# Performance work log

Measured on AMD Instinct MI355X. Metric: run time of the kernel, lower is better.

The kernel has to match this reference:

```python
import jax, jax.numpy as jnp
import numpy as np

ROPE_THETA = 10000.0

def _apply_rope(t):
    # t: [B, H, S, D]; rotate interleaved even/odd pairs
    B, H, S, D = t.shape
    inv_freq = 1.0 / (ROPE_THETA ** (jnp.arange(0, D, 2, dtype=jnp.float32) / D))  # [D/2]
    ang = jnp.arange(S, dtype=jnp.float32)[:, None] * inv_freq[None, :]            # [S, D/2]
    cos = jnp.cos(ang)[None, None]  # [1,1,S,D/2]
    sin = jnp.sin(ang)[None, None]
    te = t[..., 0::2]
    to = t[..., 1::2]
    re = te * cos - to * sin
    ro = te * sin + to * cos
    out = jnp.stack([re, ro], axis=-1).reshape(B, H, S, D)
    return out

def setup_inputs() -> dict:
    key = jax.random.key(0)
    ks = jax.random.split(key, 5)
    B, S, DIM = 2, 2048, 2048
    x = jax.random.normal(ks[0], (B, S, DIM), dtype=jnp.float32)
    scale = 0.02
    Wq = jax.random.normal(ks[1], (DIM, DIM), dtype=jnp.float32) * scale
    Wk = jax.random.normal(ks[2], (DIM, DIM), dtype=jnp.float32) * scale
    Wv = jax.random.normal(ks[3], (DIM, DIM), dtype=jnp.float32) * scale
    Wo = jax.random.normal(ks[4], (DIM, DIM), dtype=jnp.float32) * scale
    return {"x": x, "Wq": Wq, "Wk": Wk, "Wv": Wv, "Wo": Wo}

def reference(x, Wq, Wk, Wv, Wo):
    B, S, DIM = x.shape
    H = 16
    HD = DIM // H
    # nn.Linear(bias=False) with weight [out,in]: y = x @ W.T; here W stored [in,out]
    q = (x @ Wq).reshape(B, S, H, HD).transpose(0, 2, 1, 3)  # [B,H,S,HD]
    k = (x @ Wk).reshape(B, S, H, HD).transpose(0, 2, 1, 3)
    v = (x @ Wv).reshape(B, S, H, HD).transpose(0, 2, 1, 3)
    q = _apply_rope(q)
    k = _apply_rope(k)
    scores = jnp.einsum('bhqd,bhkd->bhqk', q, k) / jnp.sqrt(jnp.float32(HD))  # [B,H,S,S]
    causal = jnp.tril(jnp.ones((S, S), dtype=bool))
    scores = jnp.where(causal[None, None], scores, jnp.float32(-jnp.inf))
    attn = jax.nn.softmax(scores, axis=-1)
    out = jnp.einsum('bhqk,bhkd->bhqd', attn, v)            # [B,H,S,HD]
    out = out.transpose(0, 2, 1, 3).reshape(B, S, DIM)
    return out @ Wo  # output projection (dropout is identity in eval)
```

## Files before the change

### kernel.cpp

```cpp
#include <hip/hip_runtime.h>
#include <hip/hip_bf16.h>
#include <math.h>

typedef __bf16 bf16;
typedef __attribute__((ext_vector_type(2))) __bf16 bf16x2;
typedef __attribute__((ext_vector_type(4))) __bf16 bf16x4;
typedef __attribute__((ext_vector_type(8))) __bf16 bf16x8;
typedef __attribute__((ext_vector_type(4))) float f32x4;

#define LDS_ASYNC16(gptr, lptr)                                                        \
  __builtin_amdgcn_global_load_lds(                                                    \
      (const __attribute__((address_space(1))) void*)(gptr),                           \
      (__attribute__((address_space(3))) void*)(lptr), 16, 0, 0)

constexpr int BATCH = 2, SEQ = 2048, DIM = 2048, NH = 16, HD = 128;
constexpr float QSC = 0.12751744f;
constexpr float FREQC = 0.20762050593046f;

template <int CTRL>
__device__ __forceinline__ float dpp_mov_f(float x) {
  return __int_as_float(__builtin_amdgcn_update_dpp(
      __float_as_int(x), __float_as_int(x), CTRL, 0xf, 0xf, false));
}
__device__ __forceinline__ float rowmax16(float x) {
  x = fmaxf(x, dpp_mov_f<0x121>(x));
  x = fmaxf(x, dpp_mov_f<0x122>(x));
  x = fmaxf(x, dpp_mov_f<0x124>(x));
  x = fmaxf(x, dpp_mov_f<0x128>(x));
  return x;
}
__device__ __forceinline__ float rowsum16(float x) {
  x += dpp_mov_f<0x121>(x);
  x += dpp_mov_f<0x122>(x);
  x += dpp_mov_f<0x124>(x);
  x += dpp_mov_f<0x128>(x);
  return x;
}

__global__ void cvt_f32_to_bf16(const float4* __restrict__ in,
                                bf16x4* __restrict__ out, int n4) {
  int i = blockIdx.x * blockDim.x + threadIdx.x;
  if (i >= n4) return;
  float4 v = in[i];
  bf16x4 o;
  o[0] = (bf16)v.x; o[1] = (bf16)v.y; o[2] = (bf16)v.z; o[3] = (bf16)v.w;
  out[i] = o;
}

__global__ void transpose_w4(const float* __restrict__ W0, const float* __restrict__ W1,
                             const float* __restrict__ W2, const float* __restrict__ W3,
                             bf16* __restrict__ T0, bf16* __restrict__ T3) {
  __shared__ float tile[32][33];
  const int z = blockIdx.z;
  const float* W = (z == 0) ? W0 : (z == 1) ? W1 : (z == 2) ? W2 : W3;
  bf16* WT = (z == 3) ? T3 : (T0 + (size_t)z * DIM * DIM);
  int tx = threadIdx.x, ty = threadIdx.y;
  int bx = blockIdx.x * 32, by = blockIdx.y * 32;
#pragma unroll
  for (int j = 0; j < 32; j += 8)
    tile[ty + j][tx] = W[(size_t)(by + ty + j) * DIM + bx + tx];
  __syncthreads();
#pragma unroll
  for (int j = 0; j < 32; j += 8)
    WT[(size_t)(bx + ty + j) * DIM + by + tx] = (bf16)tile[tx][ty + j];
}

__device__ __forceinline__ void stage_half(const bf16* __restrict__ src, int g0, int ks,
                                           bf16* lds, int w, int lane) {
#pragma unroll
  for (int j = 0; j < 2; ++j) {
    const int u = (j * 8 + w) * 64 + lane;
    const int row = u >> 2;
    const int kc = (u & 3) ^ ((u >> 3) & 3);
    LDS_ASYNC16(src + (size_t)(g0 + row) * DIM + ks + kc * 8,
                lds + (size_t)((j * 8 + w) * 64) * 8);
  }
}

__global__ __launch_bounds__(512) void gemm_qkv(const bf16* __restrict__ A,
                                                const bf16* __restrict__ BT,
                                                bf16* __restrict__ Qb,
                                                bf16* __restrict__ Kb,
                                                bf16* __restrict__ VTo) {
  constexpr int RSZ = 256 * 32;
  constexpr int NT = DIM / 64;
  __shared__ __attribute__((aligned(16))) bf16 As[4 * RSZ];
  __shared__ __attribute__((aligned(16))) bf16 Bs[4 * RSZ];
  const int tid = threadIdx.x;
  const int w = tid >> 6, lane = tid & 63;
  const int quad = lane >> 4, ln = lane & 15;
  const int wm = w >> 2, wn = w & 3;
  const int lb = blockIdx.x;
  const int wgid = (lb & 7) * 48 + (lb >> 3);
  const int bx = wgid % 24, by = wgid / 24;
  const int m0 = by * 256, n0 = bx * 256;
  const int pc = (quad ^ ((ln >> 1) & 3)) * 8;
  const int aoff = wm * 128 + ln;
  const int boff = wn * 64 + ln;

  f32x4 acc[8][4] = {};

  stage_half(A,  m0, 0,  As + 0 * RSZ, w, lane);
  stage_half(BT, n0, 0,  Bs + 0 * RSZ, w, lane);
  stage_half(A,  m0, 32, As + 1 * RSZ, w, lane);
  stage_half(BT, n0, 32, Bs + 1 * RSZ, w, lane);
  stage_half(A,  m0, 64, As + 2 * RSZ, w, lane);
  stage_half(BT, n0, 64, Bs + 2 * RSZ, w, lane);
  stage_half(BT, n0, 96, Bs + 3 * RSZ, w, lane);
  asm volatile("s_waitcnt vmcnt(6)" ::: "memory");
  __builtin_amdgcn_s_barrier();

#pragma unroll 2
  for (int t = 0; t < NT; ++t) {
    const int b2 = (t & 1) * 2;
    const bf16* Ab0 = As + b2 * RSZ;
    const bf16* Ab1 = Ab0 + RSZ;
    const bf16* Bb0 = Bs + b2 * RSZ;
    const bf16* Bb1 = Bb0 + RSZ;
    bf16x8 af[4], bfr[4];

#pragma unroll
    for (int i = 0; i < 4; ++i)
      af[i] = *(const bf16x8*)(Ab0 + (aoff + i * 16) * 32 + pc);
#pragma unroll
    for (int i = 0; i < 4; ++i)
      bfr[i] = *(const bf16x8*)(Bb0 + (boff + i * 16) * 32 + pc);
    if (t + 1 < NT)
      stage_half(A, m0, (t + 1) * 64 + 32, As + ((((t + 1) & 1) * 2) + 1) * RSZ, w, lane);
    __builtin_amdgcn_s_barrier();
    asm volatile("s_waitcnt lgkmcnt(0)" ::: "memory");
    __builtin_amdgcn_s_setprio(1);
#pragma unroll
    for (int mf = 0; mf < 4; ++mf)
#pragma unroll
      for (int nf = 0; nf < 4; ++nf)
        acc[mf][nf] = __builtin_amdgcn_mfma_f32_16x16x32_bf16(
            af[mf], bfr[nf], acc[mf][nf], 0, 0, 0);
    __builtin_amdgcn_s_setprio(0);
    __builtin_amdgcn_s_barrier();

#pragma unroll
    for (int i = 0; i < 4; ++i)
      af[i] = *(const bf16x8*)(Ab0 + (aoff + 64 + i * 16) * 32 + pc);
    if (t + 2 < NT)
      stage_half(BT, n0, (t + 2) * 64, Bs + b2 * RSZ, w, lane);
    __builtin_amdgcn_s_barrier();
    asm volatile("s_waitcnt lgkmcnt(0)" ::: "memory");
    __builtin_amdgcn_s_setprio(1);
#pragma unroll
    for (int mf = 0; mf < 4; ++mf)
#pragma unroll
      for (int nf = 0; nf < 4; ++nf)
        acc[4 + mf][nf] = __builtin_amdgcn_mfma_f32_16x16x32_bf16(
            af[mf], bfr[nf], acc[4 + mf][nf], 0, 0, 0);
    __builtin_amdgcn_s_setprio(0);
    __builtin_amdgcn_s_barrier();

#pragma unroll
    for (int i = 0; i < 4; ++i)
      af[i] = *(const bf16x8*)(Ab1 + (aoff + i * 16) * 32 + pc);
#pragma unroll
    for (int i = 0; i < 4; ++i)
      bfr[i] = *(const bf16x8*)(Bb1 + (boff + i * 16) * 32 + pc);
    if (t + 2 < NT)
      stage_half(A, m0, (t + 2) * 64, As + b2 * RSZ, w, lane);
    __builtin_amdgcn_s_barrier();
    asm volatile("s_waitcnt lgkmcnt(0)" ::: "memory");
    __builtin_amdgcn_s_setprio(1);
#pragma unroll
    for (int mf = 0; mf < 4; ++mf)
#pragma unroll
      for (int nf = 0; nf < 4; ++nf)
        acc[mf][nf] = __builtin_amdgcn_mfma_f32_16x16x32_bf16(
            af[mf], bfr[nf], acc[mf][nf], 0, 0, 0);
    __builtin_amdgcn_s_setprio(0);
    __builtin_amdgcn_s_barrier();

#pragma unroll
    for (int i = 0; i < 4; ++i)
      af[i] = *(const bf16x8*)(Ab1 + (aoff + 64 + i * 16) * 32 + pc);
    if (t + 2 < NT)
      stage_half(BT, n0, (t + 2) * 64 + 32, Bs + (b2 + 1) * RSZ, w, lane);
    __builtin_amdgcn_s_barrier();
    asm volatile("s_waitcnt lgkmcnt(0)" ::: "memory");
    __builtin_amdgcn_s_setprio(1);
#pragma unroll
    for (int mf = 0; mf < 4; ++mf)
#pragma unroll
      for (int nf = 0; nf < 4; ++nf)
        acc[4 + mf][nf] = __builtin_amdgcn_mfma_f32_16x16x32_bf16(
            af[mf], bfr[nf], acc[4 + mf][nf], 0, 0, 0);
    __builtin_amdgcn_s_setprio(0);
    if (t + 2 < NT) asm volatile("s_waitcnt vmcnt(6)" ::: "memory");
    else            asm volatile("s_waitcnt vmcnt(0)" ::: "memory");
    __builtin_amdgcn_s_barrier();
  }

  const int sel = n0 >> 11;
  if (sel == 2) {
#pragma unroll
    for (int mf = 0; mf < 8; ++mf)
#pragma unroll
      for (int nf = 0; nf < 4; ++nf) {
        int gr = m0 + wm * 128 + mf * 16 + quad * 4;
        int fc = (n0 + wn * 64 + nf * 16 + ln) & 2047;
        int bb = gr >> 11, s0 = gr & (SEQ - 1);
        int h = fc >> 7, d = fc & (HD - 1);
        bf16x4 pk;
#pragma unroll
        for (int r = 0; r < 4; ++r) pk[r] = (bf16)acc[mf][nf][r];
        *(bf16x4*)(VTo + ((size_t)((bb * NH + h) * HD + d)) * SEQ + s0) = pk;
      }
  } else {
    bf16* Dst = sel ? Kb : Qb;
    const float osc = sel ? 1.0f : QSC;
#pragma unroll
    for (int nf = 0; nf < 4; ++nf) {
      int gc = n0 + wn * 64 + nf * 16 + ln;
      int fc = gc & 2047, d = fc & (HD - 1);
      float freq = exp2f(-(float)(d >> 1) * FREQC);
      bool ev = !(d & 1);
#pragma unroll
      for (int mf = 0; mf < 8; ++mf) {
#pragma unroll
        for (int r = 0; r < 4; ++r) {
          int gr = m0 + wm * 128 + mf * 16 + quad * 4 + r;
          int s = gr & (SEQ - 1);
          float ang = (float)s * freq;
          float sn, cs;
          __sincosf(ang, &sn, &cs);
          float own = acc[mf][nf][r];
          float oth = __shfl_xor(own, 1);
          float res = ev ? (own * cs - oth * sn) : (oth * sn + own * cs);
          Dst[(size_t)gr * DIM + fc] = (bf16)(res * osc);
        }
      }
    }
  }
}

template <int MODE>
__global__ __launch_bounds__(256) void gemm_bt(const bf16* __restrict__ A,
                                               const bf16* __restrict__ BT,
                                               void* __restrict__ C) {
  __shared__ __attribute__((aligned(16))) bf16 As[128 * 64];
  __shared__ __attribute__((aligned(16))) bf16 Bs[128 * 64];
  const int tid = threadIdx.x;
  const int w = tid >> 6, lane = tid & 63;
  const int quad = lane >> 4, ln = lane & 15;
  const int m0 = blockIdx.y * 128, n0 = blockIdx.x * 128;
  const int wm = (w >> 1) * 64, wn = (w & 1) * 64;
  const int l7 = ln & 7;
  f32x4 acc[4][4] = {};

  for (int k0 = 0; k0 < DIM; k0 += 64) {
#pragma unroll
    for (int i = 0; i < 4; ++i) {
      const int c = i * 256 + tid;
      const int row = c >> 3, p = c & 7;
      LDS_ASYNC16(A  + (size_t)(m0 + row) * DIM + k0 + ((p ^ (row & 7)) * 8),
                  As + (size_t)(i * 256 + w * 64) * 8);
      LDS_ASYNC16(BT + (size_t)(n0 + row) * DIM + k0 + ((p ^ (row & 7)) * 8),
                  Bs + (size_t)(i * 256 + w * 64) * 8);
    }
    __syncthreads();
#pragma unroll
    for (int kh = 0; kh < 2; ++kh) {
      bf16x8 af[4], bfr[4];
#pragma unroll
      for (int t = 0; t < 4; ++t)
        af[t] = *(const bf16x8*)(As + (wm + t * 16 + ln) * 64 +
                                 (((kh * 4 + quad) ^ l7) * 8));
#pragma unroll
      for (int t = 0; t < 4; ++t)
        bfr[t] = *(const bf16x8*)(Bs + (wn + t * 16 + ln) * 64 +
                                  (((kh * 4 + quad) ^ l7) * 8));
#pragma unroll
      for (int mt = 0; mt < 4; ++mt)
#pragma unroll
        for (int nt = 0; nt < 4; ++nt)
          acc[mt][nt] = __builtin_amdgcn_mfma_f32_16x16x32_bf16(
              af[mt], bfr[nt], acc[mt][nt], 0, 0, 0);
    }
    __syncthreads();
  }

  if (MODE == 0) {
    bf16* Co = (bf16*)C;
#pragma unroll
    for (int mt = 0; mt < 4; ++mt)
#pragma unroll
      for (int nt = 0; nt < 4; ++nt) {
        int gr = m0 + wm + mt * 16 + quad * 4;
        int gc = n0 + wn + nt * 16 + ln;
#pragma unroll
        for (int r = 0; r < 4; ++r)
          Co[(size_t)(gr + r) * DIM + gc] = (bf16)acc[mt][nt][r];
      }
  } else {
    float* Co = (float*)C;
#pragma unroll
    for (int mt = 0; mt < 4; ++mt)
#pragma unroll
      for (int nt = 0; nt < 4; ++nt) {
        int gr = m0 + wm + mt * 16 + quad * 4;
        int gc = n0 + wn + nt * 16 + ln;
#pragma unroll
        for (int r = 0; r < 4; ++r)
          Co[(size_t)(gr + r) * DIM + gc] = acc[mt][nt][r];
      }
  }
}

__device__ __forceinline__ int ml_off(int t) {
  return (t < 10) ? 2 * (t - 5) : (t < 15) ? 10 + 3 * (t - 10) : 25;
}
__device__ __forceinline__ int op_off(int t) {
  return (t < 10) ? (t - 5) : (t < 15) ? 5 + 2 * (t - 10) : 15;
}

constexpr int PSTR = 72;
__global__ __launch_bounds__(256) void flash_attn(
    const bf16* __restrict__ Q, const bf16* __restrict__ K,
    const bf16* __restrict__ VT, bf16* __restrict__ O,
    bf16* __restrict__ Opart, float* __restrict__ Mpart,
    float* __restrict__ Lpart) {
  __shared__ __attribute__((aligned(16))) bf16 Ks[64 * 128];
  __shared__ __attribute__((aligned(16))) bf16 VTs[128 * 64];
  __shared__ __attribute__((aligned(16))) bf16 Ps[4][32 * PSTR];
  const int tid = threadIdx.x;
  const int w = tid >> 6, lane = tid & 63, quad = lane >> 4, ln = lane & 15;
  const int lb = blockIdx.x;
  const int low3 = lb & 7, rest = lb >> 3;
  const int e = rest % 34;
  const int bh = (rest / 34) * 8 + low3;
  int t, c0, nc;
  if (e < 5)       { t = e;                  c0 = 0;               nc = 1; }
  else if (e < 15) { t = 5 + ((e - 5) >> 1); c0 = (e - 5) & 1;     nc = 2; }
  else if (e < 30) { int q = (e - 15) / 3;   t = 10 + q; c0 = (e - 15) - 3 * q; nc = 3; }
  else             { t = 15;                 c0 = e - 30;          nc = 4; }
  const int q0 = t * 128;
  const int ktN = 2 * (t + 1);
  const int kt0 = c0 * 10;
  const int kt1 = min(kt0 + 10, ktN);
  const bool chunked = (nc > 1);
  const int b = bh >> 4, h = bh & 15;

  bf16x8 qf[2][4];
#pragma unroll
  for (int mt = 0; mt < 2; ++mt)
#pragma unroll
    for (int kc = 0; kc < 4; ++kc)
      qf[mt][kc] = *(const bf16x8*)(Q + ((size_t)b * SEQ + q0 + w * 32 + mt * 16 + ln) * DIM +
                                    h * HD + kc * 32 + quad * 8);
  f32x4 o[2][8] = {};
  float mst[2][4], lst[2][4];
#pragma unroll
  for (int mt = 0; mt < 2; ++mt)
#pragma unroll
    for (int r = 0; r < 4; ++r) { mst[mt][r] = -1e30f; lst[mt][r] = 0.f; }

  for (int kt = kt0; kt < kt1; ++kt) {
    __syncthreads();
#pragma unroll
    for (int i = 0; i < 4; ++i) {
      const int c = i * 256 + tid;
      LDS_ASYNC16(K + ((size_t)b * SEQ + kt * 64 + (c >> 4)) * DIM + h * HD +
                      (((c & 15) ^ ((c >> 4) & 15)) * 8),
                  Ks + (size_t)(i * 256 + w * 64) * 8);
      LDS_ASYNC16(VT + ((size_t)((b * NH + h) * HD) + (c >> 3)) * SEQ + kt * 64 +
                      (((c & 7) ^ ((c >> 3) & 7)) * 8),
                  VTs + (size_t)(i * 256 + w * 64) * 8);
    }
    __syncthreads();

    f32x4 s[2][4] = {};
#pragma unroll
    for (int nt = 0; nt < 4; ++nt) {
      bf16x8 kf[4];
#pragma unroll
      for (int kc = 0; kc < 4; ++kc)
        kf[kc] = *(const bf16x8*)(Ks + (nt * 16 + ln) * 128 +
                                  (((kc * 4 + quad) ^ ln) * 8));
#pragma unroll
      for (int kc = 0; kc < 4; ++kc)
#pragma unroll
        for (int mt = 0; mt < 2; ++mt)
          s[mt][nt] = __builtin_amdgcn_mfma_f32_16x16x32_bf16(
              qf[mt][kc], kf[kc], s[mt][nt], 0, 0, 0);
    }

    const bool diag = (kt * 64 + 63 > q0);
    if (diag) {
#pragma unroll
      for (int mt = 0; mt < 2; ++mt)
#pragma unroll
        for (int nt = 0; nt < 4; ++nt)
#pragma unroll
          for (int r = 0; r < 4; ++r) {
            int kg = kt * 64 + nt * 16 + ln;
            int qg = q0 + w * 32 + mt * 16 + quad * 4 + r;
            if (kg > qg) s[mt][nt][r] = -1e30f;
          }
    }

#pragma unroll
    for (int mt = 0; mt < 2; ++mt)
#pragma unroll
      for (int r = 0; r < 4; ++r) {
        float rm = fmaxf(fmaxf(s[mt][0][r], s[mt][1][r]),
                         fmaxf(s[mt][2][r], s[mt][3][r]));
        rm = rowmax16(rm);
        float mold = mst[mt][r];
        float mnew = fmaxf(mold, rm);
        float alpha = exp2f(mold - mnew);
        mst[mt][r] = mnew;
        float rs = 0.f;
#pragma unroll
        for (int nt = 0; nt < 4; ++nt) {
          float p = exp2f(s[mt][nt][r] - mnew);
          rs += p;
          Ps[w][(mt * 16 + quad * 4 + r) * PSTR + nt * 16 + ln] = (bf16)p;
        }
        lst[mt][r] = lst[mt][r] * alpha + rs;
#pragma unroll
        for (int nd = 0; nd < 8; ++nd) o[mt][nd][r] *= alpha;
      }
    __syncthreads();

#pragma unroll
    for (int kc2 = 0; kc2 < 2; ++kc2) {
      bf16x8 pf[2];
#pragma unroll
      for (int mt = 0; mt < 2; ++mt)
        pf[mt] = *(const bf16x8*)(&Ps[w][(mt * 16 + ln) * PSTR + kc2 * 32 + quad * 8]);
#pragma unroll
      for (int nd = 0; nd < 8; ++nd) {
        bf16x8 vf = *(const bf16x8*)(VTs + (nd * 16 + ln) * 64 +
                                     (((kc2 * 4 + quad) ^ (ln & 7)) * 8));
#pragma unroll
        for (int mt = 0; mt < 2; ++mt)
          o[mt][nd] = __builtin_amdgcn_mfma_f32_16x16x32_bf16(
              pf[mt], vf, o[mt][nd], 0, 0, 0);
      }
    }
  }

  if (!chunked) {
#pragma unroll
    for (int mt = 0; mt < 2; ++mt)
#pragma unroll
      for (int r = 0; r < 4; ++r) {
        float inv = 1.f / rowsum16(lst[mt][r]);
        int qg = q0 + w * 32 + mt * 16 + quad * 4 + r;
#pragma unroll
        for (int nd = 0; nd < 8; ++nd)
          O[((size_t)b * SEQ + qg) * DIM + h * HD + nd * 16 + ln] =
              (bf16)(o[mt][nd][r] * inv);
      }
  } else {
    const int mls = bh * 29 + ml_off(t) + c0;
    bf16* Op = (c0 == 0) ? nullptr
                         : Opart + (size_t)(bh * 18 + op_off(t) + (c0 - 1)) * (128 * 128);
#pragma unroll
    for (int mt = 0; mt < 2; ++mt)
#pragma unroll
      for (int r = 0; r < 4; ++r) {
        float l = rowsum16(lst[mt][r]);
        int qr = w * 32 + mt * 16 + quad * 4 + r;
        if (ln == 0) {
          Mpart[mls * 128 + qr] = mst[mt][r];
          Lpart[mls * 128 + qr] = l;
        }
        if (c0 == 0) {
#pragma unroll
          for (int nd = 0; nd < 8; ++nd)
            O[((size_t)b * SEQ + q0 + qr) * DIM + h * HD + nd * 16 + ln] =
                (bf16)o[mt][nd][r];
        } else {
#pragma unroll
          for (int nd = 0; nd < 8; ++nd)
            Op[qr * 128 + nd * 16 + ln] = (bf16)o[mt][nd][r];
        }
      }
  }
}

__global__ __launch_bounds__(256) void flash_merge(const bf16* __restrict__ Opart,
                                                   const float* __restrict__ Mpart,
                                                   const float* __restrict__ Lpart,
                                                   bf16* __restrict__ O) {
  const int bh = blockIdx.x;
  const int t = 5 + blockIdx.y;
  const int nc = (t < 10) ? 2 : (t < 15) ? 3 : 4;
  const int b = bh >> 4, h = bh & 15;
  const int row = threadIdx.x >> 1, half = threadIdx.x & 1;
  const int mlb = bh * 29 + ml_off(t);
  float m[4], l[4], wt[4];
  float M = -1e30f;
  for (int c = 0; c < nc; ++c) {
    m[c] = Mpart[(mlb + c) * 128 + row];
    l[c] = Lpart[(mlb + c) * 128 + row];
    M = fmaxf(M, m[c]);
  }
  float wsum = 0.f;
  for (int c = 0; c < nc; ++c) { wt[c] = exp2f(m[c] - M); wsum += wt[c] * l[c]; }
  const float inv = 1.f / wsum;
  bf16* dst = O + ((size_t)b * SEQ + t * 128 + row) * DIM + h * HD + half * 64;
  const bf16* pb = Opart + (size_t)(bh * 18 + op_off(t)) * (128 * 128) + row * 128 + half * 64;
#pragma unroll
  for (int j = 0; j < 8; ++j) {
    bf16x8 a0 = *(const bf16x8*)(dst + j * 8);
    float acc[8];
#pragma unroll
    for (int k = 0; k < 8; ++k) acc[k] = wt[0] * (float)a0[k];
    for (int c = 1; c < nc; ++c) {
      bf16x8 a = *(const bf16x8*)(pb + (size_t)(c - 1) * (128 * 128) + j * 8);
#pragma unroll
      for (int k = 0; k < 8; ++k) acc[k] += wt[c] * (float)a[k];
    }
    bf16x8 o8;
#pragma unroll
    for (int k = 0; k < 8; ++k) o8[k] = (bf16)(acc[k] * inv);
    *(bf16x8*)(dst + j * 8) = o8;
  }
}

extern "C" void kernel_launch(void* const* d_in, const int* in_sizes, int n_in,
                              void* d_out, int out_size, void* d_ws, size_t ws_size,
                              hipStream_t stream) {
  (void)in_sizes; (void)n_in; (void)out_size; (void)ws_size;
  const float* x  = (const float*)d_in[0];
  const float* Wq = (const float*)d_in[1];
  const float* Wk = (const float*)d_in[2];
  const float* Wv = (const float*)d_in[3];
  const float* Wo = (const float*)d_in[4];

  char* ws = (char*)d_ws;
  const size_t MB = 1u << 20;
  const size_t WB = (size_t)DIM * DIM * 2;
  bf16* WTqkv = (bf16*)(ws);
  bf16* WoT   = (bf16*)(ws + 3 * WB);
  bf16* xb    = (bf16*)(ws + 32 * MB);
  bf16* Qb    = (bf16*)(ws + 48 * MB);
  bf16* Kb    = (bf16*)(ws + 64 * MB);
  bf16* VT    = (bf16*)(ws + 80 * MB);
  bf16* Ab    = xb;
  bf16*  Opart = (bf16*)(ws);
  float* Mpart = (float*)(ws + 19 * MB);
  float* Lpart = (float*)(ws + 19 * MB + 512 * 1024);

  int n4 = BATCH * SEQ * DIM / 4;
  cvt_f32_to_bf16<<<n4 / 256, 256, 0, stream>>>((const float4*)x, (bf16x4*)xb, n4);
  dim3 tb(32, 8), tg(DIM / 32, DIM / 32, 4);
  transpose_w4<<<tg, tb, 0, stream>>>(Wq, Wk, Wv, Wo, WTqkv, WoT);

  gemm_qkv<<<24 * 16, 512, 0, stream>>>(xb, WTqkv, Qb, Kb, VT);

  flash_attn<<<34 * BATCH * NH, 256, 0, stream>>>(Qb, Kb, VT, Ab, Opart, Mpart, Lpart);
  dim3 mg(BATCH * NH, 11);
  flash_merge<<<mg, 256, 0, stream>>>(Opart, Mpart, Lpart, Ab);

  dim3 gg(DIM / 128, BATCH * SEQ / 128);
  gemm_bt<2><<<gg, 256, 0, stream>>>(Ab, WoT, d_out);
}
```

Baseline: 458.3 us.

## Shrink QKV GEMM tile to 128x256 and remap blocks per XCD

```diff
diff --git a/kernel.cpp b/kernel.cpp
--- a/kernel.cpp
+++ b/kernel.cpp
@@ -65,8 +65,16 @@
     WT[(size_t)(bx + ty + j) * DIM + by + tx] = (bf16)tile[tx][ty + j];
 }
 
-__device__ __forceinline__ void stage_half(const bf16* __restrict__ src, int g0, int ks,
-                                           bf16* lds, int w, int lane) {
+__device__ __forceinline__ void stage_A(const bf16* __restrict__ src, int g0, int ks,
+                                        bf16* lds, int w, int lane) {
+  const int u = w * 64 + lane;
+  const int row = u >> 2;
+  const int kc = (u & 3) ^ ((u >> 3) & 3);
+  LDS_ASYNC16(src + (size_t)(g0 + row) * DIM + ks + kc * 8,
+              lds + (size_t)(w * 64) * 8);
+}
+__device__ __forceinline__ void stage_B(const bf16* __restrict__ src, int g0, int ks,
+                                        bf16* lds, int w, int lane) {
 #pragma unroll
   for (int j = 0; j < 2; ++j) {
     const int u = (j * 8 + w) * 64 + lane;
@@ -82,51 +90,55 @@
                                                 bf16* __restrict__ Qb,
                                                 bf16* __restrict__ Kb,
                                                 bf16* __restrict__ VTo) {
-  constexpr int RSZ = 256 * 32;
+  constexpr int ARSZ = 128 * 32;
+  constexpr int BRSZ = 256 * 32;
   constexpr int NT = DIM / 64;
-  __shared__ __attribute__((aligned(16))) bf16 As[4 * RSZ];
-  __shared__ __attribute__((aligned(16))) bf16 Bs[4 * RSZ];
+  __shared__ __attribute__((aligned(16))) bf16 As[4 * ARSZ];
+  __shared__ __attribute__((aligned(16))) bf16 Bs[4 * BRSZ];
   const int tid = threadIdx.x;
   const int w = tid >> 6, lane = tid & 63;
   const int quad = lane >> 4, ln = lane & 15;
   const int wm = w >> 2, wn = w & 3;
   const int lb = blockIdx.x;
-  const int wgid = (lb & 7) * 48 + (lb >> 3);
-  const int bx = wgid % 24, by = wgid / 24;
-  const int m0 = by * 256, n0 = bx * 256;
+  const int xcd = lb & 7, i = lb >> 3;
+  const int by = (xcd >> 1) * 8 + (i & 7);
+  const int bx = (xcd & 1) * 12 + (i >> 3);
+  const int m0 = by * 128, n0 = bx * 256;
   const int pc = (quad ^ ((ln >> 1) & 3)) * 8;
-  const int aoff = wm * 128 + ln;
+  const int aoff = wm * 64 + ln;
   const int boff = wn * 64 + ln;
 
-  f32x4 acc[8][4] = {};
-
-  stage_half(A,  m0, 0,  As + 0 * RSZ, w, lane);
-  stage_half(BT, n0, 0,  Bs + 0 * RSZ, w, lane);
-  stage_half(A,  m0, 32, As + 1 * RSZ, w, lane);
-  stage_half(BT, n0, 32, Bs + 1 * RSZ, w, lane);
-  stage_half(A,  m0, 64, As + 2 * RSZ, w, lane);
-  stage_half(BT, n0, 64, Bs + 2 * RSZ, w, lane);
-  stage_half(BT, n0, 96, Bs + 3 * RSZ, w, lane);
-  asm volatile("s_waitcnt vmcnt(6)" ::: "memory");
+  f32x4 acc[4][4] = {};
+
+  stage_A(A,  m0, 0,  As + 0 * ARSZ, w, lane);
+  stage_B(BT, n0, 0,  Bs + 0 * BRSZ, w, lane);
+  stage_A(A,  m0, 32, As + 1 * ARSZ, w, lane);
+  stage_B(BT, n0, 32, Bs + 1 * BRSZ, w, lane);
+  stage_A(A,  m0, 64, As + 2 * ARSZ, w, lane);
+  stage_B(BT, n0, 64, Bs + 2 * BRSZ, w, lane);
+  asm volatile("s_waitcnt vmcnt(3)" ::: "memory");
   __builtin_amdgcn_s_barrier();
 
 #pragma unroll 2
   for (int t = 0; t < NT; ++t) {
     const int b2 = (t & 1) * 2;
-    const bf16* Ab0 = As + b2 * RSZ;
-    const bf16* Ab1 = Ab0 + RSZ;
-    const bf16* Bb0 = Bs + b2 * RSZ;
-    const bf16* Bb1 = Bb0 + RSZ;
+    const bf16* Ab0 = As + b2 * ARSZ;
+    const bf16* Ab1 = Ab0 + ARSZ;
+    const bf16* Bb0 = Bs + b2 * BRSZ;
+    const bf16* Bb1 = Bb0 + BRSZ;
     bf16x8 af[4], bfr[4];
 
 #pragma unroll
-    for (int i = 0; i < 4; ++i)
-      af[i] = *(const bf16x8*)(Ab0 + (aoff + i * 16) * 32 + pc);
-#pragma unroll
-    for (int i = 0; i < 4; ++i)
-      bfr[i] = *(const bf16x8*)(Bb0 + (boff + i * 16) * 32 + pc);
-    if (t + 1 < NT)
-      stage_half(A, m0, (t + 1) * 64 + 32, As + ((((t + 1) & 1) * 2) + 1) * RSZ, w, lane);
+    for (int f = 0; f < 4; ++f)
+      af[f] = *(const bf16x8*)(Ab0 + (aoff + f * 16) * 32 + pc);
+#pragma unroll
+    for (int f = 0; f < 4; ++f)
+      bfr[f] = *(const bf16x8*)(Bb0 + (boff + f * 16) * 32 + pc);
+    if (t + 1 < NT) {
+      const int r1 = ((t + 1) & 1) * 2 + 1;
+      stage_A(A,  m0, (t + 1) * 64 + 32, As + r1 * ARSZ, w, lane);
+      stage_B(BT, n0, (t + 1) * 64 + 32, Bs + r1 * BRSZ, w, lane);
+    }
     __builtin_amdgcn_s_barrier();
     asm volatile("s_waitcnt lgkmcnt(0)" ::: "memory");
     __builtin_amdgcn_s_setprio(1);
@@ -140,30 +152,15 @@
     __builtin_amdgcn_s_barrier();
 
 #pragma unroll
-    for (int i = 0; i < 4; ++i)
-      af[i] = *(const bf16x8*)(Ab0 + (aoff + 64 + i * 16) * 32 + pc);
-    if (t + 2 < NT)
-      stage_half(BT, n0, (t + 2) * 64, Bs + b2 * RSZ, w, lane);
-    __builtin_amdgcn_s_barrier();
-    asm volatile("s_waitcnt lgkmcnt(0)" ::: "memory");
-    __builtin_amdgcn_s_setprio(1);
-#pragma unroll
-    for (int mf = 0; mf < 4; ++mf)
-#pragma unroll
-      for (int nf = 0; nf < 4; ++nf)
-        acc[4 + mf][nf] = __builtin_amdgcn_mfma_f32_16x16x32_bf16(
-            af[mf], bfr[nf], acc[4 + mf][nf], 0, 0, 0);
-    __builtin_amdgcn_s_setprio(0);
-    __builtin_amdgcn_s_barrier();
-
-#pragma unroll
-    for (int i = 0; i < 4; ++i)
-      af[i] = *(const bf16x8*)(Ab1 + (aoff + i * 16) * 32 + pc);
-#pragma unroll
-    for (int i = 0; i < 4; ++i)
-      bfr[i] = *(const bf16x8*)(Bb1 + (boff + i * 16) * 32 + pc);
-    if (t + 2 < NT)
-      stage_half(A, m0, (t + 2) * 64, As + b2 * RSZ, w, lane);
+    for (int f = 0; f < 4; ++f)
+      af[f] = *(const bf16x8*)(Ab1 + (aoff + f * 16) * 32 + pc);
+#pragma unroll
+    for (int f = 0; f < 4; ++f)
+      bfr[f] = *(const bf16x8*)(Bb1 + (boff + f * 16) * 32 + pc);
+    if (t + 2 < NT) {
+      stage_A(A,  m0, (t + 2) * 64, As + b2 * ARSZ, w, lane);
+      stage_B(BT, n0, (t + 2) * 64, Bs + b2 * BRSZ, w, lane);
+    }
     __builtin_amdgcn_s_barrier();
     asm volatile("s_waitcnt lgkmcnt(0)" ::: "memory");
     __builtin_amdgcn_s_setprio(1);
@@ -174,24 +171,7 @@
         acc[mf][nf] = __builtin_amdgcn_mfma_f32_16x16x32_bf16(
             af[mf], bfr[nf], acc[mf][nf], 0, 0, 0);
     __builtin_amdgcn_s_setprio(0);
-    __builtin_amdgcn_s_barrier();
-
-#pragma unroll
-    for (int i = 0; i < 4; ++i)
-      af[i] = *(const bf16x8*)(Ab1 + (aoff + 64 + i * 16) * 32 + pc);
-    if (t + 2 < NT)
-      stage_half(BT, n0, (t + 2) * 64 + 32, Bs + (b2 + 1) * RSZ, w, lane);
-    __builtin_amdgcn_s_barrier();
-    asm volatile("s_waitcnt lgkmcnt(0)" ::: "memory");
-    __builtin_amdgcn_s_setprio(1);
-#pragma unroll
-    for (int mf = 0; mf < 4; ++mf)
-#pragma unroll
-      for (int nf = 0; nf < 4; ++nf)
-        acc[4 + mf][nf] = __builtin_amdgcn_mfma_f32_16x16x32_bf16(
-            af[mf], bfr[nf], acc[4 + mf][nf], 0, 0, 0);
-    __builtin_amdgcn_s_setprio(0);
-    if (t + 2 < NT) asm volatile("s_waitcnt vmcnt(6)" ::: "memory");
+    if (t + 2 < NT) asm volatile("s_waitcnt vmcnt(3)" ::: "memory");
     else            asm volatile("s_waitcnt vmcnt(0)" ::: "memory");
     __builtin_amdgcn_s_barrier();
   }
@@ -199,10 +179,10 @@
   const int sel = n0 >> 11;
   if (sel == 2) {
 #pragma unroll
-    for (int mf = 0; mf < 8; ++mf)
+    for (int mf = 0; mf < 4; ++mf)
 #pragma unroll
       for (int nf = 0; nf < 4; ++nf) {
-        int gr = m0 + wm * 128 + mf * 16 + quad * 4;
+        int gr = m0 + wm * 64 + mf * 16 + quad * 4;
         int fc = (n0 + wn * 64 + nf * 16 + ln) & 2047;
         int bb = gr >> 11, s0 = gr & (SEQ - 1);
         int h = fc >> 7, d = fc & (HD - 1);
@@ -221,10 +201,10 @@
       float freq = exp2f(-(float)(d >> 1) * FREQC);
       bool ev = !(d & 1);
 #pragma unroll
-      for (int mf = 0; mf < 8; ++mf) {
+      for (int mf = 0; mf < 4; ++mf) {
 #pragma unroll
         for (int r = 0; r < 4; ++r) {
-          int gr = m0 + wm * 128 + mf * 16 + quad * 4 + r;
+          int gr = m0 + wm * 64 + mf * 16 + quad * 4 + r;
           int s = gr & (SEQ - 1);
           float ang = (float)s * freq;
           float sn, cs;
@@ -555,7 +535,7 @@
   dim3 tb(32, 8), tg(DIM / 32, DIM / 32, 4);
   transpose_w4<<<tg, tb, 0, stream>>>(Wq, Wk, Wv, Wo, WTqkv, WoT);
 
-  gemm_qkv<<<24 * 16, 512, 0, stream>>>(xb, WTqkv, Qb, Kb, VT);
+  gemm_qkv<<<768, 512, 0, stream>>>(xb, WTqkv, Qb, Kb, VT);
 
   flash_attn<<<34 * BATCH * NH, 256, 0, stream>>>(Qb, Kb, VT, Ab, Opart, Mpart, Lpart);
   dim3 mg(BATCH * NH, 11);
```

Result: faster. 442.7 us (-3.4%).
